# Performance work log

Hardware: AMD Instinct MI355X
Metric: run time of the kernel (lower is better)

The kernel has to match this reference:

```python
import jax, jax.numpy as jnp
import numpy as np

CLAMP_MIN = 1e-30
DIAG_SCALE = 10.0


def _fast_cdist(x1, x2):
    # mean-center both by x1's row-mean (as in torch source)
    adjustment = x1.mean(axis=-2, keepdims=True)
    x1 = x1 - adjustment
    x2 = x2 - adjustment
    x1_norm = jnp.sum(x1 * x1, axis=-1, keepdims=True)  # [N,1]
    x2_norm = jnp.sum(x2 * x2, axis=-1, keepdims=True)  # [N,1]
    # matmul trick: ||a-b||^2 = ||a||^2 + ||b||^2 - 2 a.b
    res = (-2.0) * (x1 @ x2.T) + x1_norm + x2_norm.T
    return jnp.sqrt(jnp.maximum(res, CLAMP_MIN))


def reference(x):
    # L2-normalize rows
    norm = jnp.linalg.norm(x, axis=-1, keepdims=True)
    x_norm = x / norm
    dist_mat = _fast_cdist(x_norm, x_norm)  # [N, N]
    d = jnp.diagonal(dist_mat)
    dist_mat = dist_mat + DIAG_SCALE * jnp.diag(1.0 - d)
    loss = jnp.max(1.0 / dist_mat, axis=1)
    return jnp.mean(loss)


def setup_inputs() -> dict:
    key = jax.random.key(0)
    x = jax.random.normal(key, (8192, 256), dtype=jnp.float32)
    return {"x": x}
```

## Files before the change

kernel.cpp:

```cpp
#include <hip/hip_runtime.h>
#include <stdint.h>

#define N_ROWS 8192
#define N_DIM  256
#define NB     64
#define NTRI   2080

typedef __attribute__((ext_vector_type(8))) short bf16x8;
typedef __attribute__((ext_vector_type(4))) float f32x4;

__device__ inline unsigned short f2bf(float f) {
    unsigned u = __float_as_uint(f);
    unsigned r = (u + 0x7FFFu + ((u >> 16) & 1u)) >> 16;
    return (unsigned short)r;
}
__device__ inline float bf2f(unsigned short b) {
    return __uint_as_float(((unsigned)b) << 16);
}
__device__ inline unsigned encf(float f) {
    unsigned u = __float_as_uint(f);
    return u ^ ((u & 0x80000000u) ? 0xFFFFFFFFu : 0x80000000u);
}
__device__ inline float decf(unsigned e) {
    unsigned u = e ^ ((e & 0x80000000u) ? 0x80000000u : 0xFFFFFFFFu);
    return __uint_as_float(u);
}
#define ENC_BIG 0xF149F2CAu

#define GLD_LDS16(g, l)                                                        \
    __builtin_amdgcn_global_load_lds(                                          \
        (const __attribute__((address_space(1))) unsigned int*)(g),            \
        (__attribute__((address_space(3))) unsigned int*)(l), 16, 0, 0)


__global__ __launch_bounds__(256) void k_norm_fast(const float* __restrict__ x,
                                                   char* __restrict__ zf,
                                                   float* __restrict__ nsq,
                                                   unsigned* __restrict__ rmin,
                                                   float* __restrict__ out) {
    if (blockIdx.x == 0 && threadIdx.x == 0) *out = 0.0f;
    const int lane = threadIdx.x & 63;
    const int w    = threadIdx.x >> 6;
    const int row  = blockIdx.x * 4 + w;
    const float4* xr = (const float4*)(x + (size_t)row * N_DIM);
    float4 v = xr[lane];
    float ss = v.x*v.x + v.y*v.y + v.z*v.z + v.w*v.w;
    #pragma unroll
    for (int m = 1; m < 64; m <<= 1) ss += __shfl_xor(ss, m, 64);
    const float inv = 1.0f / sqrtf(ss);
    unsigned short b0 = f2bf(v.x * inv);
    unsigned short b1 = f2bf(v.y * inv);
    unsigned short b2 = f2bf(v.z * inv);
    unsigned short b3 = f2bf(v.w * inv);
    ushort4 uv; uv.x = b0; uv.y = b1; uv.z = b2; uv.w = b3;
    *(ushort4*)(zf + ((size_t)(row >> 4) << 13) + ((lane >> 1) << 8) +
                ((row & 15) << 4) + ((lane & 1) << 3)) = uv;
    float z0 = bf2f(b0), z1 = bf2f(b1), z2 = bf2f(b2), z3 = bf2f(b3);
    float s2 = z0*z0 + z1*z1 + z2*z2 + z3*z3;
    #pragma unroll
    for (int m = 1; m < 64; m <<= 1) s2 += __shfl_xor(s2, m, 64);
    if (lane == 0) {
        nsq[row]  = s2;
        rmin[row] = ENC_BIG;
    }
}

__global__ __launch_bounds__(256, 3) void k_gemm_fast(const char* __restrict__ zf,
                                                      const float* __restrict__ nsq,
                                                      unsigned* __restrict__ rmin) {
    __shared__ char  As[32 * 1024];
    __shared__ float pminR[128][2];
    __shared__ float pminC[128][2];

    const int tid   = threadIdx.x;
    const int lane  = tid & 63;
    const int w     = tid >> 6;
    const int waveM = (w >> 1) * 64;
    const int waveN = (w & 1) * 64;

    const int t = blockIdx.x;
    int br = (int)((129.0f - sqrtf(16641.0f - 8.0f * (float)t)) * 0.5f);
    while ((br + 1) * (129 - (br + 1)) / 2 <= t) ++br;
    while (br * (129 - br) / 2 > t) --br;
    const int bc = br + (t - br * (129 - br) / 2);
    const bool isdiag = (br == bc);

    const char* gA    = zf + (size_t)br * 65536;
    const char* laneB = zf + ((size_t)(bc * 8 + (waveN >> 4))) * 8192 + lane * 16;

    f32x4 acc[4][4];
    #pragma unroll
    for (int m = 0; m < 4; ++m)
        #pragma unroll
        for (int n = 0; n < 4; ++n)
            acc[m][n] = (f32x4){0.f, 0.f, 0.f, 0.f};

    bf16x8 bbuf[3][4];
    #pragma unroll
    for (int n = 0; n < 4; ++n) bbuf[0][n] = *(const bf16x8*)(laneB + (size_t)n * 8192 + 0 * 1024);
    #pragma unroll
    for (int n = 0; n < 4; ++n) bbuf[1][n] = *(const bf16x8*)(laneB + (size_t)n * 8192 + 1 * 1024);

    #pragma unroll
    for (int h = 0; h < 2; ++h) {
        __syncthreads();
        #pragma unroll
        for (int c = 0; c < 8; ++c)
            GLD_LDS16(gA + (size_t)c * 8192 + h * 4096 + w * 1024 + lane * 16,
                      As + c * 4096 + w * 1024);
        __syncthreads();

        #pragma unroll
        for (int s = 0; s < 4; ++s) {
            const int g = h * 4 + s;
            if (g + 2 < 8) {
                #pragma unroll
                for (int n = 0; n < 4; ++n)
                    bbuf[(g + 2) % 3][n] =
                        *(const bf16x8*)(laneB + (size_t)n * 8192 + (g + 2) * 1024);
            }
            bf16x8 af[4];
            #pragma unroll
            for (int m = 0; m < 4; ++m)
                af[m] = *(const bf16x8*)&As[((waveM >> 4) + m) * 4096 + s * 1024 + lane * 16];
            #pragma unroll
            for (int m = 0; m < 4; ++m)
                #pragma unroll
                for (int n = 0; n < 4; ++n)
                    acc[m][n] = __builtin_amdgcn_mfma_f32_16x16x32_bf16(
                        af[m], bbuf[g % 3][n], acc[m][n], 0, 0, 0);
        }
    }

    asm volatile("" ::: "memory");

    float nj[4];
    #pragma unroll
    for (int n = 0; n < 4; ++n)
        nj[n] = nsq[bc * 128 + waveN + n * 16 + (lane & 15)];
    float4 ni4[4];
    #pragma unroll
    for (int m = 0; m < 4; ++m)
        ni4[m] = *(const float4*)&nsq[br * 128 + waveM + m * 16 + (lane >> 4) * 4];

    float rminv[4][4];
    float cminv[4];
    #pragma unroll
    for (int m = 0; m < 4; ++m)
        #pragma unroll
        for (int r = 0; r < 4; ++r)
            rminv[m][r] = 1e30f;
    #pragma unroll
    for (int n = 0; n < 4; ++n)
        cminv[n] = 1e30f;

    const int lrow0 = waveM + (lane >> 4) * 4;
    const int lcol0 = waveN + (lane & 15);
    #pragma unroll
    for (int m = 0; m < 4; ++m) {
        #pragma unroll
        for (int r = 0; r < 4; ++r) {
            const int lr = lrow0 + m * 16 + r;
            const float nir = ((const float*)&ni4[m])[r];
            #pragma unroll
            for (int n = 0; n < 4; ++n) {
                float u = fmaf(-2.0f, acc[m][n][r], nir + nj[n]);
                const bool diag = isdiag && (lr == (lcol0 + n * 16));
                u = diag ? 1e30f : u;
                rminv[m][r] = fminf(rminv[m][r], u);
                cminv[n]    = fminf(cminv[n], u);
            }
        }
    }
    #pragma unroll
    for (int mask = 1; mask < 16; mask <<= 1)
        #pragma unroll
        for (int m = 0; m < 4; ++m)
            #pragma unroll
            for (int r = 0; r < 4; ++r)
                rminv[m][r] = fminf(rminv[m][r], __shfl_xor(rminv[m][r], mask, 64));
    if ((lane & 15) == 0) {
        const int q = lane >> 4;
        #pragma unroll
        for (int m = 0; m < 4; ++m)
            #pragma unroll
            for (int r = 0; r < 4; ++r)
                pminR[waveM + m * 16 + q * 4 + r][w & 1] = rminv[m][r];
    }
    if (!isdiag) {
        #pragma unroll
        for (int mask = 16; mask < 64; mask <<= 1)
            #pragma unroll
            for (int n = 0; n < 4; ++n)
                cminv[n] = fminf(cminv[n], __shfl_xor(cminv[n], mask, 64));
        if (lane < 16) {
            #pragma unroll
            for (int n = 0; n < 4; ++n)
                pminC[waveN + n * 16 + lane][w >> 1] = cminv[n];
        }
    }
    __syncthreads();
    if (tid < 128) {
        const float v = fminf(pminR[tid][0], pminR[tid][1]);
        atomicMin(&rmin[br * 128 + tid], encf(v));
        if (!isdiag) {
            const float vc = fminf(pminC[tid][0], pminC[tid][1]);
            atomicMin(&rmin[bc * 128 + tid], encf(vc));
        }
    }
}

__global__ __launch_bounds__(256) void k_norm_fb(const float* x,
                                                 char* zb, long zstride,
                                                 char* nsqb, long nstride,
                                                 char* rminb, long rstride,
                                                 float* out) {
    if (blockIdx.x == 0 && threadIdx.x == 0) *out = 0.0f;
    const int lane = threadIdx.x & 63;
    const int w    = threadIdx.x >> 6;
    const int row  = blockIdx.x * 4 + w;
    const float4* xr = (const float4*)(x + (size_t)row * N_DIM);
    float4 v = xr[lane];
    float ss = v.x*v.x + v.y*v.y + v.z*v.z + v.w*v.w;
    #pragma unroll
    for (int m = 1; m < 64; m <<= 1) ss += __shfl_xor(ss, m, 64);
    const float inv = 1.0f / sqrtf(ss);
    unsigned short b0 = f2bf(v.x * inv), b1 = f2bf(v.y * inv);
    unsigned short b2 = f2bf(v.z * inv), b3 = f2bf(v.w * inv);
    ushort4 uv; uv.x = b0; uv.y = b1; uv.z = b2; uv.w = b3;
    *(ushort4*)(zb + (size_t)row * zstride + lane * 8) = uv;
    float z0 = bf2f(b0), z1 = bf2f(b1), z2 = bf2f(b2), z3 = bf2f(b3);
    float s2 = z0*z0 + z1*z1 + z2*z2 + z3*z3;
    #pragma unroll
    for (int m = 1; m < 64; m <<= 1) s2 += __shfl_xor(s2, m, 64);
    if (lane == 0) {
        *(float*)(nsqb + (size_t)row * nstride) = s2;
        *(unsigned*)(rminb + (size_t)row * rstride) = ENC_BIG;
    }
}

__global__ __launch_bounds__(256, 4) void k_gemm_fb(const char* zb, long zstride,
                                                    const char* nsqb, long nstride,
                                                    char* rminb, long rstride) {
    __shared__ unsigned short As[128 * 64];
    __shared__ unsigned short Bs[128 * 64];
    __shared__ float pminR[128][2];
    __shared__ float pminC[128][2];

    const int tid   = threadIdx.x;
    const int lane  = tid & 63;
    const int w     = tid >> 6;
    const int waveM = (w >> 1) * 64;
    const int waveN = (w & 1) * 64;

    const int t = blockIdx.x;
    int br = (int)((129.0f - sqrtf(16641.0f - 8.0f * (float)t)) * 0.5f);
    while ((br + 1) * (129 - (br + 1)) / 2 <= t) ++br;
    while (br * (129 - br) / 2 > t) --br;
    const int bc = br + (t - br * (129 - br) / 2);
    const bool isdiag = (br == bc);

    const char* gA = zb + (size_t)br * 128 * zstride;
    const char* gB = zb + (size_t)bc * 128 * zstride;

    f32x4 acc[4][4];
    #pragma unroll
    for (int m = 0; m < 4; ++m)
        #pragma unroll
        for (int n = 0; n < 4; ++n)
            acc[m][n] = (f32x4){0.f, 0.f, 0.f, 0.f};

    for (int kk = 0; kk < 4; ++kk) {
        __syncthreads();
        #pragma unroll
        for (int c = 0; c < 4; ++c) {
            const int f    = c * 4096 + tid * 16;
            const int row  = f >> 7;
            const int slot = (f >> 4) & 7;
            const int c_g  = slot ^ (row & 7);
            GLD_LDS16(gA + (size_t)row * zstride + kk * 128 + c_g * 16,
                      (char*)As + c * 4096 + w * 1024);
            GLD_LDS16(gB + (size_t)row * zstride + kk * 128 + c_g * 16,
                      (char*)Bs + c * 4096 + w * 1024);
        }
        __syncthreads();

        #pragma unroll
        for (int s = 0; s < 2; ++s) {
            bf16x8 af[4], bfr[4];
            const int q = (lane >> 4) + s * 4;
            #pragma unroll
            for (int m = 0; m < 4; ++m) {
                const int rr = waveM + m * 16 + (lane & 15);
                af[m] = *(const bf16x8*)&As[rr * 64 + ((q ^ (rr & 7)) << 3)];
            }
            #pragma unroll
            for (int n = 0; n < 4; ++n) {
                const int rr = waveN + n * 16 + (lane & 15);
                bfr[n] = *(const bf16x8*)&Bs[rr * 64 + ((q ^ (rr & 7)) << 3)];
            }
            #pragma unroll
            for (int m = 0; m < 4; ++m)
                #pragma unroll
                for (int n = 0; n < 4; ++n)
                    acc[m][n] = __builtin_amdgcn_mfma_f32_16x16x32_bf16(af[m], bfr[n], acc[m][n], 0, 0, 0);
        }
    }

    asm volatile("" ::: "memory");

    float nj[4];
    #pragma unroll
    for (int n = 0; n < 4; ++n)
        nj[n] = *(const float*)(nsqb + (size_t)(bc * 128 + waveN + n * 16 + (lane & 15)) * nstride);
    float4 ni4[4];
    #pragma unroll
    for (int m = 0; m < 4; ++m) {
        const int row0 = br * 128 + waveM + m * 16 + (lane >> 4) * 4;
        ni4[m].x = *(const float*)(nsqb + (size_t)(row0 + 0) * nstride);
        ni4[m].y = *(const float*)(nsqb + (size_t)(row0 + 1) * nstride);
        ni4[m].z = *(const float*)(nsqb + (size_t)(row0 + 2) * nstride);
        ni4[m].w = *(const float*)(nsqb + (size_t)(row0 + 3) * nstride);
    }

    float rminv[4][4];
    float cminv[4];
    #pragma unroll
    for (int m = 0; m < 4; ++m)
        #pragma unroll
        for (int r = 0; r < 4; ++r)
            rminv[m][r] = 1e30f;
    #pragma unroll
    for (int n = 0; n < 4; ++n)
        cminv[n] = 1e30f;

    const int lrow0 = waveM + (lane >> 4) * 4;
    const int lcol0 = waveN + (lane & 15);
    #pragma unroll
    for (int m = 0; m < 4; ++m) {
        #pragma unroll
        for (int r = 0; r < 4; ++r) {
            const int lr = lrow0 + m * 16 + r;
            const float nir = ((const float*)&ni4[m])[r];
            #pragma unroll
            for (int n = 0; n < 4; ++n) {
                float u = fmaf(-2.0f, acc[m][n][r], nir + nj[n]);
                const bool diag = isdiag && (lr == (lcol0 + n * 16));
                u = diag ? 1e30f : u;
                rminv[m][r] = fminf(rminv[m][r], u);
                cminv[n]    = fminf(cminv[n], u);
            }
        }
    }
    #pragma unroll
    for (int mask = 1; mask < 16; mask <<= 1)
        #pragma unroll
        for (int m = 0; m < 4; ++m)
            #pragma unroll
            for (int r = 0; r < 4; ++r)
                rminv[m][r] = fminf(rminv[m][r], __shfl_xor(rminv[m][r], mask, 64));
    if ((lane & 15) == 0) {
        const int q = lane >> 4;
        #pragma unroll
        for (int m = 0; m < 4; ++m)
            #pragma unroll
            for (int r = 0; r < 4; ++r)
                pminR[waveM + m * 16 + q * 4 + r][w & 1] = rminv[m][r];
    }
    if (!isdiag) {
        #pragma unroll
        for (int mask = 16; mask < 64; mask <<= 1)
            #pragma unroll
            for (int n = 0; n < 4; ++n)
                cminv[n] = fminf(cminv[n], __shfl_xor(cminv[n], mask, 64));
        if (lane < 16) {
            #pragma unroll
            for (int n = 0; n < 4; ++n)
                pminC[waveN + n * 16 + lane][w >> 1] = cminv[n];
        }
    }
    __syncthreads();
    if (tid < 128) {
        const float v = fminf(pminR[tid][0], pminR[tid][1]);
        atomicMin((unsigned*)(rminb + (size_t)(br * 128 + tid) * rstride), encf(v));
        if (!isdiag) {
            const float vc = fminf(pminC[tid][0], pminC[tid][1]);
            atomicMin((unsigned*)(rminb + (size_t)(bc * 128 + tid) * rstride), encf(vc));
        }
    }
}

__global__ __launch_bounds__(256) void k_final(const char* nsqb, long nstride,
                                               const char* rminb, long rstride,
                                               float* out) {
    const int r = blockIdx.x * 256 + threadIdx.x;
    const float mn  = decf(*(const unsigned*)(rminb + (size_t)r * rstride));
    const float res = fmaxf(mn, 1e-30f);
    float loss = fmaxf(1.0f / sqrtf(res), 0.1f);
    #pragma unroll
    for (int m = 1; m < 64; m <<= 1) loss += __shfl_xor(loss, m, 64);
    __shared__ float wsum[4];
    const int lane = threadIdx.x & 63, w = threadIdx.x >> 6;
    if (lane == 0) wsum[w] = loss;
    __syncthreads();
    if (threadIdx.x == 0)
        atomicAdd(out, (wsum[0] + wsum[1] + wsum[2] + wsum[3]) * (1.0f / 8192.0f));
}

extern "C" void kernel_launch(void* const* d_in, const int* in_sizes, int n_in,
                              void* d_out, int out_size, void* d_ws, size_t ws_size,
                              hipStream_t stream) {
    float* x   = (float*)d_in[0];
    float* out = (float*)d_out;
    char*  ws  = (char*)d_ws;

    const size_t WS_NEED = 4u * 1024 * 1024 + 64 * 1024 + 4096;
    if (ws_size >= WS_NEED) {
        char*     zf   = ws;
        float*    nsq  = (float*)(ws + 4u * 1024 * 1024);
        unsigned* rmin = (unsigned*)(ws + 4u * 1024 * 1024 + 32 * 1024);
        k_norm_fast<<<N_ROWS / 4, 256, 0, stream>>>(x, zf, nsq, rmin, out);
        k_gemm_fast<<<NTRI, 256, 0, stream>>>(zf, nsq, rmin);
        k_final<<<N_ROWS / 256, 256, 0, stream>>>((const char*)nsq, 4,
                                                  (const char*)rmin, 4, out);
    } else {
        char* zb    = (char*)x;       long zstride = 1024;
        char* nsqb  = (char*)x + 512; long nstride = 1024;
        char* rminb = (char*)x + 516; long rstride = 1024;
        k_norm_fb<<<N_ROWS / 4, 256, 0, stream>>>(x, zb, zstride, nsqb, nstride, rminb, rstride, out);
        k_gemm_fb<<<NTRI, 256, 0, stream>>>(zb, zstride, nsqb, nstride, rminb, rstride);
        k_final<<<N_ROWS / 256, 256, 0, stream>>>(nsqb, nstride, rminb, rstride, out);
    }
}
```

Measured before the change: 88.94 us.

## Quantize normalized rows to FP8 e4m3 and use FP8 MFMA for Gram matrix

The normalized rows are stored as FP8 e4m3 instead of bf16, halving the workspace and the global/LDS traffic for the triangular Gram GEMM. The GEMM uses fp8 MFMA instructions and now loads the whole K=256 A tile into shared memory in one pass, removing the two-stage sync loop. Occupancy launch bounds are raised from 3 to 4 blocks. The risk is precision: e4m3 has only 3 mantissa bits, so distances near the minimum (max of 1/dist) may shift and change the loss beyond tolerance, even though squared norms are recomputed from the quantized values.

```diff
diff --git a/kernel.cpp b/kernel.cpp
--- a/kernel.cpp
+++ b/kernel.cpp
@@ -1,4 +1,5 @@
 #include <hip/hip_runtime.h>
+#include <hip/hip_fp8.h>
 #include <stdint.h>
 
 #define N_ROWS 8192
@@ -48,14 +49,13 @@
     #pragma unroll
     for (int m = 1; m < 64; m <<= 1) ss += __shfl_xor(ss, m, 64);
     const float inv = 1.0f / sqrtf(ss);
-    unsigned short b0 = f2bf(v.x * inv);
-    unsigned short b1 = f2bf(v.y * inv);
-    unsigned short b2 = f2bf(v.z * inv);
-    unsigned short b3 = f2bf(v.w * inv);
-    ushort4 uv; uv.x = b0; uv.y = b1; uv.z = b2; uv.w = b3;
-    *(ushort4*)(zf + ((size_t)(row >> 4) << 13) + ((lane >> 1) << 8) +
-                ((row & 15) << 4) + ((lane & 1) << 3)) = uv;
-    float z0 = bf2f(b0), z1 = bf2f(b1), z2 = bf2f(b2), z3 = bf2f(b3);
+    __hip_fp8_e4m3 q0(v.x * inv), q1(v.y * inv), q2(v.z * inv), q3(v.w * inv);
+    unsigned packed = (unsigned)q0.__x | ((unsigned)q1.__x << 8) |
+                      ((unsigned)q2.__x << 16) | ((unsigned)q3.__x << 24);
+    const int k0 = lane * 4;
+    *(unsigned*)(zf + ((size_t)(row >> 4) << 12) + ((k0 >> 5) << 9) +
+                 (((k0 >> 3) & 3) << 7) + ((row & 15) << 3) + (k0 & 7)) = packed;
+    float z0 = (float)q0, z1 = (float)q1, z2 = (float)q2, z3 = (float)q3;
     float s2 = z0*z0 + z1*z1 + z2*z2 + z3*z3;
     #pragma unroll
     for (int m = 1; m < 64; m <<= 1) s2 += __shfl_xor(s2, m, 64);
@@ -65,7 +65,7 @@
     }
 }
 
-__global__ __launch_bounds__(256, 3) void k_gemm_fast(const char* __restrict__ zf,
+__global__ __launch_bounds__(256, 4) void k_gemm_fast(const char* __restrict__ zf,
                                                       const float* __restrict__ nsq,
                                                       unsigned* __restrict__ rmin) {
     __shared__ char  As[32 * 1024];
@@ -85,8 +85,8 @@
     const int bc = br + (t - br * (129 - br) / 2);
     const bool isdiag = (br == bc);
 
-    const char* gA    = zf + (size_t)br * 65536;
-    const char* laneB = zf + ((size_t)(bc * 8 + (waveN >> 4))) * 8192 + lane * 16;
+    const char* gA    = zf + (size_t)br * 32768;
+    const char* laneB = zf + ((size_t)(bc * 8 + (waveN >> 4))) * 4096 + lane * 8;
 
     f32x4 acc[4][4];
     #pragma unroll
@@ -95,41 +95,37 @@
         for (int n = 0; n < 4; ++n)
             acc[m][n] = (f32x4){0.f, 0.f, 0.f, 0.f};
 
-    bf16x8 bbuf[3][4];
-    #pragma unroll
-    for (int n = 0; n < 4; ++n) bbuf[0][n] = *(const bf16x8*)(laneB + (size_t)n * 8192 + 0 * 1024);
-    #pragma unroll
-    for (int n = 0; n < 4; ++n) bbuf[1][n] = *(const bf16x8*)(laneB + (size_t)n * 8192 + 1 * 1024);
-
-    #pragma unroll
-    for (int h = 0; h < 2; ++h) {
-        __syncthreads();
-        #pragma unroll
-        for (int c = 0; c < 8; ++c)
-            GLD_LDS16(gA + (size_t)c * 8192 + h * 4096 + w * 1024 + lane * 16,
-                      As + c * 4096 + w * 1024);
-        __syncthreads();
-
-        #pragma unroll
-        for (int s = 0; s < 4; ++s) {
-            const int g = h * 4 + s;
-            if (g + 2 < 8) {
-                #pragma unroll
-                for (int n = 0; n < 4; ++n)
-                    bbuf[(g + 2) % 3][n] =
-                        *(const bf16x8*)(laneB + (size_t)n * 8192 + (g + 2) * 1024);
-            }
-            bf16x8 af[4];
-            #pragma unroll
-            for (int m = 0; m < 4; ++m)
-                af[m] = *(const bf16x8*)&As[((waveM >> 4) + m) * 4096 + s * 1024 + lane * 16];
-            #pragma unroll
-            for (int m = 0; m < 4; ++m)
-                #pragma unroll
-                for (int n = 0; n < 4; ++n)
-                    acc[m][n] = __builtin_amdgcn_mfma_f32_16x16x32_bf16(
-                        af[m], bbuf[g % 3][n], acc[m][n], 0, 0, 0);
-        }
+    #pragma unroll
+    for (int c = 0; c < 8; ++c)
+        GLD_LDS16(gA + (size_t)c * 4096 + w * 1024 + lane * 16,
+                  As + c * 4096 + w * 1024);
+
+    long bbuf[3][4];
+    #pragma unroll
+    for (int n = 0; n < 4; ++n) bbuf[0][n] = *(const long*)(laneB + (size_t)n * 4096 + 0 * 512);
+    #pragma unroll
+    for (int n = 0; n < 4; ++n) bbuf[1][n] = *(const long*)(laneB + (size_t)n * 4096 + 1 * 512);
+
+    __syncthreads();
+
+    #pragma unroll
+    for (int g = 0; g < 8; ++g) {
+        if (g + 2 < 8) {
+            #pragma unroll
+            for (int n = 0; n < 4; ++n)
+                bbuf[(g + 2) % 3][n] =
+                    *(const long*)(laneB + (size_t)n * 4096 + (g + 2) * 512);
+        }
+        long af[4];
+        #pragma unroll
+        for (int m = 0; m < 4; ++m)
+            af[m] = *(const long*)&As[((waveM >> 4) + m) * 4096 + g * 512 + lane * 8];
+        #pragma unroll
+        for (int m = 0; m < 4; ++m)
+            #pragma unroll
+            for (int n = 0; n < 4; ++n)
+                acc[m][n] = __builtin_amdgcn_mfma_f32_16x16x32_fp8_fp8(
+                    af[m], bbuf[g % 3][n], acc[m][n], 0, 0, 0);
     }
 
     asm volatile("" ::: "memory");
@@ -414,11 +410,11 @@
     float* out = (float*)d_out;
     char*  ws  = (char*)d_ws;
 
-    const size_t WS_NEED = 4u * 1024 * 1024 + 64 * 1024 + 4096;
+    const size_t WS_NEED = 2u * 1024 * 1024 + 64 * 1024 + 4096;
     if (ws_size >= WS_NEED) {
         char*     zf   = ws;
-        float*    nsq  = (float*)(ws + 4u * 1024 * 1024);
-        unsigned* rmin = (unsigned*)(ws + 4u * 1024 * 1024 + 32 * 1024);
+        float*    nsq  = (float*)(ws + 2u * 1024 * 1024);
+        unsigned* rmin = (unsigned*)(ws + 2u * 1024 * 1024 + 32 * 1024);
         k_norm_fast<<<N_ROWS / 4, 256, 0, stream>>>(x, zf, nsq, rmin, out);
         k_gemm_fast<<<NTRI, 256, 0, stream>>>(zf, nsq, rmin);
         k_final<<<N_ROWS / 256, 256, 0, stream>>>((const char*)nsq, 4,
```

Result: faster. 81.36 us (median of 2 runs) (-8.5%).
